# Performance work log

Hardware: AMD Instinct MI355X
Metric: run time of the kernel (lower is better)

The kernel has to match this reference:

```python
import jax, jax.numpy as jnp
import numpy as np

N, D, H, E, TOP_K = 4096, 1024, 4096, 8, 2


def setup_inputs() -> dict:
    key = jax.random.key(0)
    ks = jax.random.split(key, 12)
    s_in = 1.0 / np.sqrt(D)
    s_hid = 1.0 / np.sqrt(H)
    return {
        "x": jax.random.normal(ks[0], (N, D), dtype=jnp.float32),
        "gate_w": jax.random.uniform(ks[1], (D, E), jnp.float32, -s_in, s_in),
        "gate_b": jax.random.uniform(ks[2], (E,), jnp.float32, -s_in, s_in),
        "w1": jax.random.uniform(ks[3], (E, D, H), jnp.float32, -s_in, s_in),
        "b1": jax.random.uniform(ks[4], (E, H), jnp.float32, -s_in, s_in),
        "w2": jax.random.uniform(ks[5], (E, H, D), jnp.float32, -s_hid, s_hid),
        "b2": jax.random.uniform(ks[6], (E, D), jnp.float32, -s_hid, s_hid),
        "sw1": jax.random.uniform(ks[7], (D, H), jnp.float32, -s_in, s_in),
        "sb1": jax.random.uniform(ks[8], (H,), jnp.float32, -s_in, s_in),
        "sw2": jax.random.uniform(ks[9], (H, D), jnp.float32, -s_hid, s_hid),
        "sb2": jax.random.uniform(ks[10], (D,), jnp.float32, -s_hid, s_hid),
    }


def reference(x, gate_w, gate_b, w1, b1, w2, b2, sw1, sb1, sw2, sb2):
    # Gating
    gate_logits = x @ gate_w + gate_b                      # [N, E]
    gate_probs = jax.nn.softmax(gate_logits, axis=-1)      # [N, E]
    top_logits, selected = jax.lax.top_k(gate_logits, TOP_K)  # [N, K]
    top_w = jax.nn.softmax(top_logits, axis=-1).astype(x.dtype)
    # Dense combine weights: [N, E], zero for unselected experts
    combine = (jax.nn.one_hot(selected, E, dtype=x.dtype) * top_w[..., None]).sum(axis=1)
    # All-expert FFN (exact GELU like torch nn.GELU default)
    h = jax.nn.gelu(jnp.einsum('nd,edh->enh', x, w1) + b1[:, None, :], approximate=False)
    y = jnp.einsum('enh,ehd->end', h, w2) + b2[:, None, :]  # [E, N, D]
    results = jnp.einsum('end,ne->nd', y, combine)
    # Shared expert
    sh = jax.nn.gelu(x @ sw1 + sb1, approximate=False)
    results = results + sh @ sw2 + sb2
    # Aux load-balancing loss
    importance = gate_probs.sum(axis=0)                     # [E]
    load = jax.nn.one_hot(selected, E, dtype=jnp.float32).sum(axis=(0, 1))
    importance = importance / (importance.sum() + 1e-8)
    load = load / (load.sum() + 1e-8)
    aux_loss = jnp.sum((importance - load) ** 2)
    return results, aux_loss
```

## Files before the change

kernel.cpp:

```cpp
#include <hip/hip_runtime.h>
#include <hip/hip_bf16.h>

#define N_TOK 4096
#define DIM   1024
#define HID   4096
#define NE    8
#define ROW_CAP128 13312
#define ROW_CAP64  12800

typedef unsigned short ushort_t;
typedef short bf16x8 __attribute__((ext_vector_type(8)));
typedef float f32x4 __attribute__((ext_vector_type(4)));

__device__ __forceinline__ ushort_t f2bf(float f) {
    unsigned int u = __float_as_uint(f);
    u += 0x7fffu + ((u >> 16) & 1u);
    return (ushort_t)(u >> 16);
}
__device__ __forceinline__ float bf2f(ushort_t u) {
    return __uint_as_float(((unsigned int)u) << 16);
}
__device__ __forceinline__ float gelu_f(float v) {
    return 0.5f * v * (1.0f + erff(v * 0.70710678118654752f));
}
__device__ __forceinline__ void async_load16(const void* g, void* l) {
    __builtin_amdgcn_global_load_lds(
        (const __attribute__((address_space(1))) void*)g,
        (__attribute__((address_space(3))) void*)l, 16, 0, 0);
}
__device__ __forceinline__ void fma4x4(const float4& a, const float4& b, float acc[4][4]) {
    acc[0][0] = fmaf(a.x, b.x, acc[0][0]); acc[0][1] = fmaf(a.x, b.y, acc[0][1]);
    acc[0][2] = fmaf(a.x, b.z, acc[0][2]); acc[0][3] = fmaf(a.x, b.w, acc[0][3]);
    acc[1][0] = fmaf(a.y, b.x, acc[1][0]); acc[1][1] = fmaf(a.y, b.y, acc[1][1]);
    acc[1][2] = fmaf(a.y, b.z, acc[1][2]); acc[1][3] = fmaf(a.y, b.w, acc[1][3]);
    acc[2][0] = fmaf(a.z, b.x, acc[2][0]); acc[2][1] = fmaf(a.z, b.y, acc[2][1]);
    acc[2][2] = fmaf(a.z, b.z, acc[2][2]); acc[2][3] = fmaf(a.z, b.w, acc[2][3]);
    acc[3][0] = fmaf(a.w, b.x, acc[3][0]); acc[3][1] = fmaf(a.w, b.y, acc[3][1]);
    acc[3][2] = fmaf(a.w, b.z, acc[3][2]); acc[3][3] = fmaf(a.w, b.w, acc[3][3]);
}

__global__ __launch_bounds__(256) void gate_kernel(
    const float* __restrict__ x, const float* __restrict__ gw, const float* __restrict__ gb,
    int* __restrict__ counts, float* __restrict__ importance,
    int* __restrict__ sel, float* __restrict__ selw)
{
    __shared__ float s_imp[NE];
    __shared__ int   s_cnt[NE];
    int tid = threadIdx.x;
    if (tid < NE) { s_imp[tid] = 0.f; s_cnt[tid] = 0; }
    __syncthreads();

    int wave = tid >> 6, lane = tid & 63;
    int n = blockIdx.x * 4 + wave;

    float acc[NE];
#pragma unroll
    for (int e = 0; e < NE; ++e) acc[e] = 0.f;

    const float* xr = x + (size_t)n * DIM;
    for (int it = 0; it < DIM / 64; ++it) {
        int d = it * 64 + lane;
        float xv = xr[d];
        const float4* g = (const float4*)(gw + (size_t)d * NE);
        float4 g0 = g[0], g1 = g[1];
        acc[0] = fmaf(xv, g0.x, acc[0]); acc[1] = fmaf(xv, g0.y, acc[1]);
        acc[2] = fmaf(xv, g0.z, acc[2]); acc[3] = fmaf(xv, g0.w, acc[3]);
        acc[4] = fmaf(xv, g1.x, acc[4]); acc[5] = fmaf(xv, g1.y, acc[5]);
        acc[6] = fmaf(xv, g1.z, acc[6]); acc[7] = fmaf(xv, g1.w, acc[7]);
    }
#pragma unroll
    for (int off = 32; off > 0; off >>= 1) {
#pragma unroll
        for (int e = 0; e < NE; ++e) acc[e] += __shfl_down(acc[e], off, 64);
    }

    if (lane == 0) {
        float lg[NE], p[NE];
        float mx = -1e30f;
#pragma unroll
        for (int e = 0; e < NE; ++e) { lg[e] = acc[e] + gb[e]; mx = fmaxf(mx, lg[e]); }
        float se = 0.f;
#pragma unroll
        for (int e = 0; e < NE; ++e) { p[e] = expf(lg[e] - mx); se += p[e]; }
        float inv = 1.f / se;
#pragma unroll
        for (int e = 0; e < NE; ++e) atomicAdd(&s_imp[e], p[e] * inv);
        int i1 = 0;
#pragma unroll
        for (int e = 1; e < NE; ++e) if (lg[e] > lg[i1]) i1 = e;
        int i2 = -1;
#pragma unroll
        for (int e = 0; e < NE; ++e) if (e != i1 && (i2 < 0 || lg[e] > lg[i2])) i2 = e;
        float t = expf(lg[i2] - lg[i1]);
        float wA = 1.f / (1.f + t), wB = t / (1.f + t);
        sel[n * 2] = i1; sel[n * 2 + 1] = i2;
        selw[n * 2] = wA; selw[n * 2 + 1] = wB;
        atomicAdd(&s_cnt[i1], 1); atomicAdd(&s_cnt[i2], 1);
    }
    __syncthreads();
    if (tid < NE) {
        atomicAdd(&importance[tid], s_imp[tid]);
        atomicAdd(&counts[tid], s_cnt[tid]);
    }
}

__global__ void plan_kernel(
    const int* __restrict__ counts, const float* __restrict__ importance,
    int* __restrict__ cursors, int* __restrict__ offs, int* __restrict__ total_rows,
    int* __restrict__ row_token, float* __restrict__ row_wt, float* __restrict__ out_aux,
    int al)
{
    __shared__ int s_offs[NE + 1], s_cnt[NE];
    if (threadIdx.x == 0) {
        int o = 0;
        for (int e = 0; e < NE; ++e) {
            s_cnt[e] = counts[e];
            s_offs[e] = o;
            cursors[e] = o;
            o += (s_cnt[e] + al - 1) & ~(al - 1);
        }
        s_offs[NE] = o;
        for (int e = 0; e <= NE; ++e) offs[e] = s_offs[e];
        *total_rows = o + N_TOK;
        float is = 1e-8f, ls = 1e-8f;
        for (int e = 0; e < NE; ++e) { is += importance[e]; ls += (float)s_cnt[e]; }
        float aux = 0.f;
        for (int e = 0; e < NE; ++e) {
            float d = importance[e] / is - (float)s_cnt[e] / ls;
            aux += d * d;
        }
        *out_aux = aux;
    }
    __syncthreads();
    for (int e = 0; e < NE; ++e) {
        int st = s_offs[e] + s_cnt[e], en = s_offs[e + 1];
        for (int i = st + (int)threadIdx.x; i < en; i += (int)blockDim.x) {
            row_token[i] = -1; row_wt[i] = 0.f;
        }
    }
}

__global__ __launch_bounds__(256) void scatter_kernel(
    const int* __restrict__ sel, const float* __restrict__ selw,
    int* __restrict__ cursors, const int* __restrict__ offs,
    int* __restrict__ row_token, float* __restrict__ row_wt)
{
    int n = blockIdx.x * 256 + threadIdx.x;
#pragma unroll
    for (int k = 0; k < 2; ++k) {
        int e = sel[n * 2 + k];
        int pos = atomicAdd(&cursors[e], 1);
        row_token[pos] = n;
        row_wt[pos] = selw[n * 2 + k];
    }
    int off8 = offs[NE];
    row_token[off8 + n] = n;
    row_wt[off8 + n] = 1.0f;
}

__global__ __launch_bounds__(256) void cvt_x_kernel(
    const float* __restrict__ x, ushort_t* __restrict__ xb)
{
    int i = (blockIdx.x * 256 + threadIdx.x) * 8;
    float4 a = *(const float4*)(x + i);
    float4 b = *(const float4*)(x + i + 4);
    uint4 o;
    o.x = ((unsigned)f2bf(a.y) << 16) | f2bf(a.x);
    o.y = ((unsigned)f2bf(a.w) << 16) | f2bf(a.z);
    o.z = ((unsigned)f2bf(b.y) << 16) | f2bf(b.x);
    o.w = ((unsigned)f2bf(b.w) << 16) | f2bf(b.z);
    *(uint4*)(xb + i) = o;
}

__global__ __launch_bounds__(256) void transpose_bf16(
    const float* __restrict__ src, const float* __restrict__ srcS,
    ushort_t* __restrict__ dst, int K, int N)
{
    __shared__ ushort_t T[64][80];
    const float* s = (blockIdx.z < 8) ? (src + (size_t)blockIdx.z * K * N) : srcS;
    dst += (size_t)blockIdx.z * K * N;
    int n0 = blockIdx.x * 64, k0 = blockIdx.y * 64;
    int t = threadIdx.x;
    int cq = (t & 15) * 4;
    int kr = t >> 4;
#pragma unroll
    for (int rI = 0; rI < 4; ++rI) {
        int k = kr + rI * 16;
        float4 v = *(const float4*)(s + (size_t)(k0 + k) * N + n0 + cq);
        T[cq + 0][k] = f2bf(v.x);
        T[cq + 1][k] = f2bf(v.y);
        T[cq + 2][k] = f2bf(v.z);
        T[cq + 3][k] = f2bf(v.w);
    }
    __syncthreads();
    int nr = t >> 2;
    int kq = (t & 3) * 16;
    uint4 o0 = *(const uint4*)&T[nr][kq];
    uint4 o1 = *(const uint4*)&T[nr][kq + 8];
    ushort_t* dp = dst + (size_t)(n0 + nr) * K + k0 + kq;
    *(uint4*)dp = o0;
    *(uint4*)(dp + 8) = o1;
}

__global__ __launch_bounds__(256) void ffn1_mfma(
    const ushort_t* __restrict__ xb, const ushort_t* __restrict__ wtbuf,
    const float* __restrict__ b1, const float* __restrict__ sb1,
    const int* __restrict__ offs, const int* __restrict__ total_rows,
    const int* __restrict__ row_token, ushort_t* __restrict__ hbuf)
{
    const int row0 = blockIdx.y * 128;
    if (row0 >= *total_rows) return;
    const int col0 = blockIdx.x * 128;

    int e = 0;
#pragma unroll
    for (int i = 0; i < NE; ++i) e += (row0 >= offs[i + 1]) ? 1 : 0;
    const ushort_t* W = wtbuf + (size_t)e * (HID * DIM);
    const float* Bv = (e < NE) ? (b1 + (size_t)e * HID) : sb1;

    __shared__ ushort_t As[4096];
    __shared__ ushort_t Bs[4096];

    const int tid = threadIdx.x;
    const int lane = tid & 63;
    const int w = tid >> 6;
    const int wm = w & 1, wn = w >> 1;
    const int lm = lane & 15, lk = lane >> 4;

    const int sS = 2 * w;
    int r0 = row0 + (sS + 0) * 16 + lm;
    int r1 = row0 + (sS + 1) * 16 + lm;
    int t0 = row_token[r0]; if (t0 < 0) t0 = 0;
    int t1 = row_token[r1]; if (t1 < 0) t1 = 0;
    const ushort_t* gA0 = xb + (size_t)t0 * DIM + lk * 8;
    const ushort_t* gA1 = xb + (size_t)t1 * DIM + lk * 8;
    const ushort_t* gB0 = W + (size_t)(col0 + (sS + 0) * 16 + lm) * DIM + lk * 8;
    const ushort_t* gB1 = W + (size_t)(col0 + (sS + 1) * 16 + lm) * DIM + lk * 8;
    ushort_t* lA0 = &As[(sS + 0) * 512];
    ushort_t* lA1 = &As[(sS + 1) * 512];
    ushort_t* lB0 = &Bs[(sS + 0) * 512];
    ushort_t* lB1 = &Bs[(sS + 1) * 512];

    f32x4 zero = {0.f, 0.f, 0.f, 0.f};
    f32x4 acc[4][4];
#pragma unroll
    for (int i = 0; i < 4; ++i)
#pragma unroll
        for (int j = 0; j < 4; ++j) acc[i][j] = zero;

    const bf16x8* Af = (const bf16x8*)As;
    const bf16x8* Bf = (const bf16x8*)Bs;

    for (int k0 = 0; k0 < DIM; k0 += 32) {
        async_load16(gA0 + k0, lA0);
        async_load16(gA1 + k0, lA1);
        async_load16(gB0 + k0, lB0);
        async_load16(gB1 + k0, lB1);
        __syncthreads();
        bf16x8 a[4], b[4];
#pragma unroll
        for (int i = 0; i < 4; ++i) a[i] = Af[(wm * 4 + i) * 64 + lane];
#pragma unroll
        for (int j = 0; j < 4; ++j) b[j] = Bf[(wn * 4 + j) * 64 + lane];
#pragma unroll
        for (int i = 0; i < 4; ++i)
#pragma unroll
            for (int j = 0; j < 4; ++j)
                acc[i][j] = __builtin_amdgcn_mfma_f32_16x16x32_bf16(a[i], b[j], acc[i][j], 0, 0, 0);
        __syncthreads();
    }

#pragma unroll
    for (int j = 0; j < 4; ++j) {
        int C = col0 + (wn * 4 + j) * 16 + lm;
        float bj = Bv[C];
#pragma unroll
        for (int i = 0; i < 4; ++i) {
            int Rb = row0 + (wm * 4 + i) * 16 + lk * 4;
#pragma unroll
            for (int r = 0; r < 4; ++r) {
                float v = gelu_f(acc[i][j][r] + bj);
                hbuf[(size_t)(Rb + r) * HID + C] = f2bf(v);
            }
        }
    }
}

__global__ __launch_bounds__(256) void ffn2_mfma(
    const ushort_t* __restrict__ hbuf, const ushort_t* __restrict__ wtbuf,
    const float* __restrict__ b2, const float* __restrict__ sb2,
    const int* __restrict__ offs, const int* __restrict__ total_rows,
    const int* __restrict__ row_token, const float* __restrict__ row_wt,
    float* __restrict__ out)
{
    const int row0 = blockIdx.y * 128;
    if (row0 >= *total_rows) return;
    const int col0 = blockIdx.x * 128;
    const int kc = blockIdx.z;
    const int kLo = kc * (HID / 2), kHi = kLo + (HID / 2);

    int e = 0;
#pragma unroll
    for (int i = 0; i < NE; ++i) e += (row0 >= offs[i + 1]) ? 1 : 0;
    const ushort_t* W = wtbuf + (size_t)e * (HID * DIM);
    const float* Bv = (e < NE) ? (b2 + (size_t)e * DIM) : sb2;

    __shared__ ushort_t As[4096];
    __shared__ ushort_t Bs[4096];
    __shared__ int   s_tok[128];
    __shared__ float s_wt[128];

    const int tid = threadIdx.x;
    if (tid < 128) { s_tok[tid] = row_token[row0 + tid]; s_wt[tid] = row_wt[row0 + tid]; }

    const int lane = tid & 63;
    const int w = tid >> 6;
    const int wm = w & 1, wn = w >> 1;
    const int lm = lane & 15, lk = lane >> 4;

    const int sS = 2 * w;
    const ushort_t* gA0 = hbuf + (size_t)(row0 + (sS + 0) * 16 + lm) * HID + lk * 8;
    const ushort_t* gA1 = hbuf + (size_t)(row0 + (sS + 1) * 16 + lm) * HID + lk * 8;
    const ushort_t* gB0 = W + (size_t)(col0 + (sS + 0) * 16 + lm) * HID + lk * 8;
    const ushort_t* gB1 = W + (size_t)(col0 + (sS + 1) * 16 + lm) * HID + lk * 8;
    ushort_t* lA0 = &As[(sS + 0) * 512];
    ushort_t* lA1 = &As[(sS + 1) * 512];
    ushort_t* lB0 = &Bs[(sS + 0) * 512];
    ushort_t* lB1 = &Bs[(sS + 1) * 512];

    f32x4 zero = {0.f, 0.f, 0.f, 0.f};
    f32x4 acc[4][4];
#pragma unroll
    for (int i = 0; i < 4; ++i)
#pragma unroll
        for (int j = 0; j < 4; ++j) acc[i][j] = zero;

    const bf16x8* Af = (const bf16x8*)As;
    const bf16x8* Bf = (const bf16x8*)Bs;

    for (int k0 = kLo; k0 < kHi; k0 += 32) {
        async_load16(gA0 + k0, lA0);
        async_load16(gA1 + k0, lA1);
        async_load16(gB0 + k0, lB0);
        async_load16(gB1 + k0, lB1);
        __syncthreads();
        bf16x8 a[4], b[4];
#pragma unroll
        for (int i = 0; i < 4; ++i) a[i] = Af[(wm * 4 + i) * 64 + lane];
#pragma unroll
        for (int j = 0; j < 4; ++j) b[j] = Bf[(wn * 4 + j) * 64 + lane];
#pragma unroll
        for (int i = 0; i < 4; ++i)
#pragma unroll
            for (int j = 0; j < 4; ++j)
                acc[i][j] = __builtin_amdgcn_mfma_f32_16x16x32_bf16(a[i], b[j], acc[i][j], 0, 0, 0);
        __syncthreads();
    }

#pragma unroll
    for (int j = 0; j < 4; ++j) {
        int C = col0 + (wn * 4 + j) * 16 + lm;
        float bj = (kc == 0) ? Bv[C] : 0.f;
#pragma unroll
        for (int i = 0; i < 4; ++i) {
            int rb = (wm * 4 + i) * 16 + lk * 4;
#pragma unroll
            for (int r = 0; r < 4; ++r) {
                int tok = s_tok[rb + r];
                if (tok < 0) continue;
                float v = s_wt[rb + r] * (acc[i][j][r] + bj);
                atomicAdd(&out[(size_t)tok * DIM + C], v);
            }
        }
    }
}

__global__ __launch_bounds__(256) void ffn1_kernel(
    const float* __restrict__ x, const float* __restrict__ w1, const float* __restrict__ b1,
    const float* __restrict__ sw1, const float* __restrict__ sb1,
    const int* __restrict__ offs, const int* __restrict__ total_rows,
    const int* __restrict__ row_token, ushort_t* __restrict__ hbuf)
{
    int row0 = blockIdx.x * 64;
    if (row0 >= *total_rows) return;
    int col0 = blockIdx.y * 64;
    int e = 0;
#pragma unroll
    for (int i = 1; i <= NE; ++i) if (row0 >= offs[i]) e = i;
    const float* W = (e < NE) ? w1 + (size_t)e * DIM * HID : sw1;
    const float* B = (e < NE) ? b1 + (size_t)e * HID : sb1;

    __shared__ float As_[16][68];
    __shared__ float Bs_[16][64];
    __shared__ int toks[64];
    int tid = threadIdx.x;
    if (tid < 64) toks[tid] = row_token[row0 + tid];
    __syncthreads();

    int am = tid >> 2, ak = (tid & 3) << 2;
    int bkr = tid >> 4, bn = (tid & 15) << 2;
    int tx = tid & 15, ty = tid >> 4;
    int tok = toks[am];
    const float* ap = x + (size_t)(tok >= 0 ? tok : 0) * DIM + ak;
    const float* bp = W + (size_t)bkr * HID + col0 + bn;

    float acc[4][4] = {};
    for (int k0 = 0; k0 < DIM; k0 += 16) {
        float4 av = make_float4(0.f, 0.f, 0.f, 0.f);
        if (tok >= 0) av = *(const float4*)(ap + k0);
        float4 bv = *(const float4*)(bp + (size_t)k0 * HID);
        As_[ak + 0][am] = av.x; As_[ak + 1][am] = av.y;
        As_[ak + 2][am] = av.z; As_[ak + 3][am] = av.w;
        *(float4*)&Bs_[bkr][bn] = bv;
        __syncthreads();
#pragma unroll
        for (int kk = 0; kk < 16; ++kk) {
            float4 a = *(const float4*)&As_[kk][ty * 4];
            float4 b = *(const float4*)&Bs_[kk][tx * 4];
            fma4x4(a, b, acc);
        }
        __syncthreads();
    }
    float4 bb = *(const float4*)(B + col0 + tx * 4);
    ushort_t* hp = hbuf + (size_t)(row0 + ty * 4) * HID + col0 + tx * 4;
#pragma unroll
    for (int r = 0; r < 4; ++r) {
        ushort4 pk;
        pk.x = f2bf(gelu_f(acc[r][0] + bb.x));
        pk.y = f2bf(gelu_f(acc[r][1] + bb.y));
        pk.z = f2bf(gelu_f(acc[r][2] + bb.z));
        pk.w = f2bf(gelu_f(acc[r][3] + bb.w));
        *(ushort4*)(hp + (size_t)r * HID) = pk;
    }
}

__global__ __launch_bounds__(256) void ffn2_kernel(
    const ushort_t* __restrict__ hbuf,
    const float* __restrict__ w2, const float* __restrict__ b2,
    const float* __restrict__ sw2, const float* __restrict__ sb2,
    const int* __restrict__ offs, const int* __restrict__ total_rows,
    const int* __restrict__ row_token, const float* __restrict__ row_wt,
    float* __restrict__ out)
{
    int row0 = blockIdx.x * 64;
    if (row0 >= *total_rows) return;
    int col0 = blockIdx.y * 64;
    int e = 0;
#pragma unroll
    for (int i = 1; i <= NE; ++i) if (row0 >= offs[i]) e = i;
    const float* W = (e < NE) ? w2 + (size_t)e * HID * DIM : sw2;
    const float* B = (e < NE) ? b2 + (size_t)e * DIM : sb2;

    __shared__ float As_[16][68];
    __shared__ float Bs_[16][64];
    __shared__ int toks[64];
    __shared__ float wts[64];
    int tid = threadIdx.x;
    if (tid < 64) { toks[tid] = row_token[row0 + tid]; wts[tid] = row_wt[row0 + tid]; }
    __syncthreads();

    int am = tid >> 2, ak = (tid & 3) << 2;
    int bkr = tid >> 4, bn = (tid & 15) << 2;
    int tx = tid & 15, ty = tid >> 4;
    const ushort_t* ap = hbuf + (size_t)(row0 + am) * HID + ak;
    const float* bp = W + (size_t)bkr * DIM + col0 + bn;

    float acc[4][4] = {};
    for (int k0 = 0; k0 < HID; k0 += 16) {
        ushort4 hv = *(const ushort4*)(ap + k0);
        float4 bv = *(const float4*)(bp + (size_t)k0 * DIM);
        As_[ak + 0][am] = bf2f(hv.x); As_[ak + 1][am] = bf2f(hv.y);
        As_[ak + 2][am] = bf2f(hv.z); As_[ak + 3][am] = bf2f(hv.w);
        *(float4*)&Bs_[bkr][bn] = bv;
        __syncthreads();
#pragma unroll
        for (int kk = 0; kk < 16; ++kk) {
            float4 a = *(const float4*)&As_[kk][ty * 4];
            float4 b = *(const float4*)&Bs_[kk][tx * 4];
            fma4x4(a, b, acc);
        }
        __syncthreads();
    }
    float4 bb = *(const float4*)(B + col0 + tx * 4);
#pragma unroll
    for (int r = 0; r < 4; ++r) {
        int rr = ty * 4 + r;
        int tok = toks[rr];
        if (tok < 0) continue;
        float w = wts[rr];
        float* op = out + (size_t)tok * DIM + col0 + tx * 4;
        atomicAdd(&op[0], w * (acc[r][0] + bb.x));
        atomicAdd(&op[1], w * (acc[r][1] + bb.y));
        atomicAdd(&op[2], w * (acc[r][2] + bb.z));
        atomicAdd(&op[3], w * (acc[r][3] + bb.w));
    }
}

extern "C" void kernel_launch(void* const* d_in, const int* in_sizes, int n_in,
                              void* d_out, int out_size, void* d_ws, size_t ws_size,
                              hipStream_t stream)
{
    const float* x   = (const float*)d_in[0];
    const float* gw  = (const float*)d_in[1];
    const float* gb  = (const float*)d_in[2];
    const float* w1  = (const float*)d_in[3];
    const float* b1  = (const float*)d_in[4];
    const float* w2  = (const float*)d_in[5];
    const float* b2  = (const float*)d_in[6];
    const float* sw1 = (const float*)d_in[7];
    const float* sb1 = (const float*)d_in[8];
    const float* sw2 = (const float*)d_in[9];
    const float* sb2 = (const float*)d_in[10];
    float* out = (float*)d_out;

    char* ws = (char*)d_ws;
    int*   counts     = (int*)(ws + 0);
    int*   cursors    = (int*)(ws + 32);
    int*   offs       = (int*)(ws + 64);
    int*   total_rows = (int*)(ws + 100);
    float* importance = (float*)(ws + 128);
    int*   sel        = (int*)(ws + 256);
    float* selw       = (float*)(ws + 33024);
    int*   row_token  = (int*)(ws + 65792);
    float* row_wt     = (float*)(ws + 119040);

    const size_t XB_OFF = 262144;
    const size_t WT_OFF = XB_OFF + (size_t)N_TOK * DIM * 2;
    const size_t HB_OFF = WT_OFF + (size_t)9 * HID * DIM * 2;
    const size_t NEED   = HB_OFF + (size_t)ROW_CAP128 * HID * 2;
    ushort_t* xb    = (ushort_t*)(ws + XB_OFF);
    ushort_t* wtbuf = (ushort_t*)(ws + WT_OFF);

    hipMemsetAsync(d_out, 0, (size_t)out_size * sizeof(float), stream);
    hipMemsetAsync(d_ws, 0, 256, stream);

    gate_kernel<<<N_TOK / 4, 256, 0, stream>>>(x, gw, gb, counts, importance, sel, selw);

    if (ws_size >= NEED) {
        ushort_t* hbuf = (ushort_t*)(ws + HB_OFF);
        plan_kernel<<<1, 64, 0, stream>>>(counts, importance, cursors, offs, total_rows,
                                          row_token, row_wt, out + (size_t)N_TOK * DIM, 128);
        scatter_kernel<<<N_TOK / 256, 256, 0, stream>>>(sel, selw, cursors, offs, row_token, row_wt);
        cvt_x_kernel<<<(N_TOK * DIM) / 2048, 256, 0, stream>>>(x, xb);
        transpose_bf16<<<dim3(HID / 64, DIM / 64, 9), 256, 0, stream>>>(w1, sw1, wtbuf, DIM, HID);
        ffn1_mfma<<<dim3(HID / 128, ROW_CAP128 / 128), 256, 0, stream>>>(
            xb, wtbuf, b1, sb1, offs, total_rows, row_token, hbuf);
        transpose_bf16<<<dim3(DIM / 64, HID / 64, 9), 256, 0, stream>>>(w2, sw2, wtbuf, HID, DIM);
        ffn2_mfma<<<dim3(DIM / 128, ROW_CAP128 / 128, 2), 256, 0, stream>>>(
            hbuf, wtbuf, b2, sb2, offs, total_rows, row_token, row_wt, out);
    } else {
        ushort_t* hbuf = (ushort_t*)(ws + 262144);
        plan_kernel<<<1, 64, 0, stream>>>(counts, importance, cursors, offs, total_rows,
                                          row_token, row_wt, out + (size_t)N_TOK * DIM, 64);
        scatter_kernel<<<N_TOK / 256, 256, 0, stream>>>(sel, selw, cursors, offs, row_token, row_wt);
        ffn1_kernel<<<dim3(ROW_CAP64 / 64, HID / 64), 256, 0, stream>>>(
            x, w1, b1, sw1, sb1, offs, total_rows, row_token, hbuf);
        ffn2_kernel<<<dim3(ROW_CAP64 / 64, DIM / 64), 256, 0, stream>>>(
            hbuf, w2, b2, sw2, sb2, offs, total_rows, row_token, row_wt, out);
    }
}
```

Baseline: 968.7 us.

## Register-prefetch next K tile in MFMA GEMMs and drop ffn2 split-K

Replaces the direct global-to-LDS async loads in both MFMA GEMM kernels with register-staged prefetch. The next K slice is loaded into registers while the current one is computed, and a barrier that waits only on LDS lets those global loads stay in flight across the sync. The ffn2 kernel also drops its two-way split-K, so each block covers the full hidden dimension, which halves the atomic adds into the output. The cost is fewer ffn2 blocks in flight (about 104×8 instead of twice that) and extra registers for the prefetch buffers.

```diff
diff --git a/kernel.cpp b/kernel.cpp
--- a/kernel.cpp
+++ b/kernel.cpp
@@ -23,10 +23,9 @@
 __device__ __forceinline__ float gelu_f(float v) {
     return 0.5f * v * (1.0f + erff(v * 0.70710678118654752f));
 }
-__device__ __forceinline__ void async_load16(const void* g, void* l) {
-    __builtin_amdgcn_global_load_lds(
-        (const __attribute__((address_space(1))) void*)g,
-        (__attribute__((address_space(3))) void*)l, 16, 0, 0);
+__device__ __forceinline__ void barrier_novm() {
+    __builtin_amdgcn_s_waitcnt(0xC07F);
+    __builtin_amdgcn_s_barrier();
 }
 __device__ __forceinline__ void fma4x4(const float4& a, const float4& b, float acc[4][4]) {
     acc[0][0] = fmaf(a.x, b.x, acc[0][0]); acc[0][1] = fmaf(a.x, b.y, acc[0][1]);
@@ -236,10 +235,10 @@
     const ushort_t* gA1 = xb + (size_t)t1 * DIM + lk * 8;
     const ushort_t* gB0 = W + (size_t)(col0 + (sS + 0) * 16 + lm) * DIM + lk * 8;
     const ushort_t* gB1 = W + (size_t)(col0 + (sS + 1) * 16 + lm) * DIM + lk * 8;
-    ushort_t* lA0 = &As[(sS + 0) * 512];
-    ushort_t* lA1 = &As[(sS + 1) * 512];
-    ushort_t* lB0 = &Bs[(sS + 0) * 512];
-    ushort_t* lB1 = &Bs[(sS + 1) * 512];
+    ushort_t* lA0 = &As[(sS + 0) * 512 + lane * 8];
+    ushort_t* lA1 = &As[(sS + 1) * 512 + lane * 8];
+    ushort_t* lB0 = &Bs[(sS + 0) * 512 + lane * 8];
+    ushort_t* lB1 = &Bs[(sS + 1) * 512 + lane * 8];
 
     f32x4 zero = {0.f, 0.f, 0.f, 0.f};
     f32x4 acc[4][4];
@@ -251,12 +250,23 @@
     const bf16x8* Af = (const bf16x8*)As;
     const bf16x8* Bf = (const bf16x8*)Bs;
 
+    uint4 rA0 = *(const uint4*)(gA0);
+    uint4 rA1 = *(const uint4*)(gA1);
+    uint4 rB0 = *(const uint4*)(gB0);
+    uint4 rB1 = *(const uint4*)(gB1);
+
     for (int k0 = 0; k0 < DIM; k0 += 32) {
-        async_load16(gA0 + k0, lA0);
-        async_load16(gA1 + k0, lA1);
-        async_load16(gB0 + k0, lB0);
-        async_load16(gB1 + k0, lB1);
+        *(uint4*)lA0 = rA0;
+        *(uint4*)lA1 = rA1;
+        *(uint4*)lB0 = rB0;
+        *(uint4*)lB1 = rB1;
         __syncthreads();
+        if (k0 + 32 < DIM) {
+            rA0 = *(const uint4*)(gA0 + k0 + 32);
+            rA1 = *(const uint4*)(gA1 + k0 + 32);
+            rB0 = *(const uint4*)(gB0 + k0 + 32);
+            rB1 = *(const uint4*)(gB1 + k0 + 32);
+        }
         bf16x8 a[4], b[4];
 #pragma unroll
         for (int i = 0; i < 4; ++i) a[i] = Af[(wm * 4 + i) * 64 + lane];
@@ -267,7 +277,7 @@
 #pragma unroll
             for (int j = 0; j < 4; ++j)
                 acc[i][j] = __builtin_amdgcn_mfma_f32_16x16x32_bf16(a[i], b[j], acc[i][j], 0, 0, 0);
-        __syncthreads();
+        barrier_novm();
     }
 
 #pragma unroll
@@ -296,8 +306,6 @@
     const int row0 = blockIdx.y * 128;
     if (row0 >= *total_rows) return;
     const int col0 = blockIdx.x * 128;
-    const int kc = blockIdx.z;
-    const int kLo = kc * (HID / 2), kHi = kLo + (HID / 2);
 
     int e = 0;
 #pragma unroll
@@ -323,10 +331,10 @@
     const ushort_t* gA1 = hbuf + (size_t)(row0 + (sS + 1) * 16 + lm) * HID + lk * 8;
     const ushort_t* gB0 = W + (size_t)(col0 + (sS + 0) * 16 + lm) * HID + lk * 8;
     const ushort_t* gB1 = W + (size_t)(col0 + (sS + 1) * 16 + lm) * HID + lk * 8;
-    ushort_t* lA0 = &As[(sS + 0) * 512];
-    ushort_t* lA1 = &As[(sS + 1) * 512];
-    ushort_t* lB0 = &Bs[(sS + 0) * 512];
-    ushort_t* lB1 = &Bs[(sS + 1) * 512];
+    ushort_t* lA0 = &As[(sS + 0) * 512 + lane * 8];
+    ushort_t* lA1 = &As[(sS + 1) * 512 + lane * 8];
+    ushort_t* lB0 = &Bs[(sS + 0) * 512 + lane * 8];
+    ushort_t* lB1 = &Bs[(sS + 1) * 512 + lane * 8];
 
     f32x4 zero = {0.f, 0.f, 0.f, 0.f};
     f32x4 acc[4][4];
@@ -338,12 +346,23 @@
     const bf16x8* Af = (const bf16x8*)As;
     const bf16x8* Bf = (const bf16x8*)Bs;
 
-    for (int k0 = kLo; k0 < kHi; k0 += 32) {
-        async_load16(gA0 + k0, lA0);
-        async_load16(gA1 + k0, lA1);
-        async_load16(gB0 + k0, lB0);
-        async_load16(gB1 + k0, lB1);
+    uint4 rA0 = *(const uint4*)(gA0);
+    uint4 rA1 = *(const uint4*)(gA1);
+    uint4 rB0 = *(const uint4*)(gB0);
+    uint4 rB1 = *(const uint4*)(gB1);
+
+    for (int k0 = 0; k0 < HID; k0 += 32) {
+        *(uint4*)lA0 = rA0;
+        *(uint4*)lA1 = rA1;
+        *(uint4*)lB0 = rB0;
+        *(uint4*)lB1 = rB1;
         __syncthreads();
+        if (k0 + 32 < HID) {
+            rA0 = *(const uint4*)(gA0 + k0 + 32);
+            rA1 = *(const uint4*)(gA1 + k0 + 32);
+            rB0 = *(const uint4*)(gB0 + k0 + 32);
+            rB1 = *(const uint4*)(gB1 + k0 + 32);
+        }
         bf16x8 a[4], b[4];
 #pragma unroll
         for (int i = 0; i < 4; ++i) a[i] = Af[(wm * 4 + i) * 64 + lane];
@@ -354,13 +373,13 @@
 #pragma unroll
             for (int j = 0; j < 4; ++j)
                 acc[i][j] = __builtin_amdgcn_mfma_f32_16x16x32_bf16(a[i], b[j], acc[i][j], 0, 0, 0);
-        __syncthreads();
+        barrier_novm();
     }
 
 #pragma unroll
     for (int j = 0; j < 4; ++j) {
         int C = col0 + (wn * 4 + j) * 16 + lm;
-        float bj = (kc == 0) ? Bv[C] : 0.f;
+        float bj = Bv[C];
 #pragma unroll
         for (int i = 0; i < 4; ++i) {
             int rb = (wm * 4 + i) * 16 + lk * 4;
@@ -546,7 +565,7 @@
         ffn1_mfma<<<dim3(HID / 128, ROW_CAP128 / 128), 256, 0, stream>>>(
             xb, wtbuf, b1, sb1, offs, total_rows, row_token, hbuf);
         transpose_bf16<<<dim3(DIM / 64, HID / 64, 9), 256, 0, stream>>>(w2, sw2, wtbuf, HID, DIM);
-        ffn2_mfma<<<dim3(DIM / 128, ROW_CAP128 / 128, 2), 256, 0, stream>>>(
+        ffn2_mfma<<<dim3(DIM / 128, ROW_CAP128 / 128), 256, 0, stream>>>(
             hbuf, wtbuf, b2, sb2, offs, total_rows, row_token, row_wt, out);
     } else {
         ushort_t* hbuf = (ushort_t*)(ws + 262144);
```

New measurement: 971.4 us. Within noise of the previous version (+0.3%).
